# Kernel tuning notes

Measured on AMD Instinct MI355X. Metric: run time of the kernel, lower is better.

## Reference

```python
import jax, jax.numpy as jnp
import numpy as np

D_MODEL = 1024
NUM_HEADS = 16
THETA = 10000.0


def _trunc_normal(key, shape):
    # matches torch.nn.init.trunc_normal_(std=std, a=-3*std, b=3*std)
    std = (2.0 / (shape[0] + shape[1])) ** 0.5
    return jax.random.truncated_normal(key, -3.0, 3.0, shape, dtype=jnp.float32) * std


def setup_inputs() -> dict:
    key = jax.random.key(0)
    kx, kq, kk, kv, ko = jax.random.split(key, 5)
    B, S, D = 2, 2048, D_MODEL
    return {
        "x": jax.random.normal(kx, (B, S, D), dtype=jnp.float32),
        "Wq": _trunc_normal(kq, (D, D)),  # torch Linear weight: [out, in]
        "Wk": _trunc_normal(kk, (D, D)),
        "Wv": _trunc_normal(kv, (D, D)),
        "Wo": _trunc_normal(ko, (D, D)),
        "token_positions": jnp.arange(S, dtype=jnp.int32),
    }


def _rope(x, token_positions):
    # x: [B, H, S, d_k]; RoPE on interleaved pairs (k r) with r=2
    d_k = x.shape[-1]
    inv_freq = THETA ** (-2.0 * jnp.arange(d_k // 2, dtype=jnp.float32) / d_k)
    ang = token_positions.astype(jnp.float32)[:, None] * inv_freq[None, :]  # [S, d_k/2]
    sin, cos = jnp.sin(ang).astype(x.dtype), jnp.cos(ang).astype(x.dtype)
    x0, x1 = x[..., 0::2], x[..., 1::2]
    y0 = x0 * cos - x1 * sin
    y1 = x0 * sin + x1 * cos
    return jnp.stack([y0, y1], axis=-1).reshape(x.shape)


def reference(x, Wq, Wk, Wv, Wo, token_positions):
    B, S, D = x.shape
    H = NUM_HEADS
    d_k = D // H

    def proj(W):  # y = x @ W^T, split heads -> [B, H, S, d_k]
        y = jnp.einsum('bsd,ed->bse', x, W)
        return y.reshape(B, S, H, d_k).transpose(0, 2, 1, 3)

    q = _rope(proj(Wq), token_positions)
    k = _rope(proj(Wk), token_positions)
    v = proj(Wv)

    # causal mask: attend where pos_k <= pos_q
    mask = token_positions[None, :] <= token_positions[:, None]  # [S_q, S_k]
    logits = jnp.einsum('bhqd,bhkd->bhqk', q, k) / (d_k ** 0.5)
    logits = jnp.where(mask, logits, -jnp.inf)
    scores = jax.nn.softmax(logits, axis=-1)
    attn = jnp.einsum('bhqk,bhkd->bhqd', scores, v)  # [B, H, S, d_k]
    attn = attn.transpose(0, 2, 1, 3).reshape(B, S, D)
    return jnp.einsum('bsd,ed->bse', attn, Wo)
```

## Files before the change

kernel.cpp:

```cpp
#include <hip/hip_runtime.h>
#include <hip/hip_bf16.h>

typedef __attribute__((ext_vector_type(8))) short s16x8;
typedef __attribute__((ext_vector_type(4))) float f32x4;

__device__ __forceinline__ unsigned short f2b(float x) {
  unsigned int u = __float_as_uint(x);
  u = (u + 0x7fffu + ((u >> 16) & 1u)) >> 16;
  return (unsigned short)u;
}

__device__ __forceinline__ float b2f(unsigned short u) {
  return __uint_as_float((unsigned int)u << 16);
}

__device__ __forceinline__ unsigned int cvtpk(float a, float b) {
  unsigned int r;
  asm("v_cvt_pk_bf16_f32 %0, %1, %2" : "=v"(r) : "v"(a), "v"(b));
  return r;
}

#if __has_builtin(__builtin_amdgcn_exp2f)
__device__ __forceinline__ float fexp2(float x) { return __builtin_amdgcn_exp2f(x); }
#else
__device__ __forceinline__ float fexp2(float x) { return exp2f(x); }
#endif

__device__ __forceinline__ void gl2lds16(const unsigned short* g, unsigned short* lds) {
  __builtin_amdgcn_global_load_lds(
      (const __attribute__((address_space(1))) unsigned int*)g,
      (__attribute__((address_space(3))) unsigned int*)lds, 16, 0, 0);
}

#define QSCALE 0.18033688011f

__global__ __launch_bounds__(256) void cast_all(
    const float* __restrict__ x,  const float* __restrict__ Wq,
    const float* __restrict__ Wk, const float* __restrict__ Wv,
    const float* __restrict__ Wo, unsigned short* __restrict__ dst,
    float2* __restrict__ tbl) {
  const int blk = blockIdx.x;
  if (blk >= 8192) {
    int idx = (blk - 8192) * 256 + threadIdx.x;
    int s = idx >> 5, d2 = idx & 31;
    float inv = __expf(-0.2878231366f * (float)d2);
    float ang = (float)s * inv;
    float sn, cs;
    __sincosf(ang, &sn, &cs);
    tbl[idx] = make_float2(cs, sn);
    return;
  }
  int i = blk * 256 + threadIdx.x;
  const float* src;
  int off;
  if (i < 1048576) { src = x; off = i; }
  else {
    int j = i - 1048576;
    int seg = j >> 18;
    off = j & 262143;
    src = (seg == 0) ? Wq : (seg == 1) ? Wk : (seg == 2) ? Wv : Wo;
  }
  const float4 v = ((const float4*)src)[off];
  uint2 o;
  o.x = cvtpk(v.x, v.y);
  o.y = cvtpk(v.z, v.w);
  ((uint2*)dst)[i] = o;
}

#define KDIM 1024

__global__ __launch_bounds__(256, 4) void gemm_qkv(
    const unsigned short* __restrict__ A,
    const unsigned short* __restrict__ Bt,
    const int* __restrict__ tok,
    unsigned short* __restrict__ Qo,
    unsigned short* __restrict__ Ko,
    unsigned short* __restrict__ Vt,
    const float2* __restrict__ tbl) {
  __shared__ unsigned short As[2][128 * 32];
  __shared__ unsigned short Bs[2][128 * 32];
  const int tid = threadIdx.x;
  const int bid = blockIdx.x;
  const int xcd = bid & 7;
  const int loc = bid >> 3;
  const int m0 = (loc / 3) * 128;
  const int n0 = (xcd * 3 + loc % 3) * 128;
  const int w = tid >> 6, lane = tid & 63;
  const int ln = lane & 15, quad = lane >> 4;
  const int wm = (w >> 1) * 64, wn = (w & 1) * 64;

  const int rr = lane >> 2;
  const int gsw = ((lane & 3) ^ ((rr ^ (rr >> 2)) & 3)) * 8;
  const int sr = (ln ^ (ln >> 2)) & 3;

  const f32x4 zero = {0.f, 0.f, 0.f, 0.f};
  f32x4 acc[4][4];
#pragma unroll
  for (int i = 0; i < 4; ++i)
#pragma unroll
    for (int j = 0; j < 4; ++j) acc[i][j] = zero;

#define QKV_STAGE(kb, p)                                                              \
  do {                                                                                \
    int col = (kb) * 32 + gsw;                                                        \
    gl2lds16(A  + (size_t)(m0 + w * 32 + rr) * KDIM + col,      &As[p][(w * 32) * 32]);      \
    gl2lds16(A  + (size_t)(m0 + w * 32 + 16 + rr) * KDIM + col, &As[p][(w * 32 + 16) * 32]); \
    gl2lds16(Bt + (size_t)(n0 + w * 32 + rr) * KDIM + col,      &Bs[p][(w * 32) * 32]);      \
    gl2lds16(Bt + (size_t)(n0 + w * 32 + 16 + rr) * KDIM + col, &Bs[p][(w * 32 + 16) * 32]); \
  } while (0)

  QKV_STAGE(0, 0);
  for (int kb = 0; kb < 32; ++kb) {
    const int p = kb & 1;
    __syncthreads();
    if (kb < 31) QKV_STAGE(kb + 1, p ^ 1);
    s16x8 af[4], bfr[4];
#pragma unroll
    for (int i = 0; i < 4; ++i)
      af[i] = *(const s16x8*)(&As[p][(wm + i * 16 + ln) * 32 + ((quad ^ sr) * 8)]);
#pragma unroll
    for (int j = 0; j < 4; ++j)
      bfr[j] = *(const s16x8*)(&Bs[p][(wn + j * 16 + ln) * 32 + ((quad ^ sr) * 8)]);
#pragma unroll
    for (int i = 0; i < 4; ++i)
#pragma unroll
      for (int j = 0; j < 4; ++j)
        acc[i][j] = __builtin_amdgcn_mfma_f32_16x16x32_bf16(af[i], bfr[j], acc[i][j], 0, 0, 0);
  }
#undef QKV_STAGE

  const bool isV = (n0 >= 2048);
  if (!isV) {
    const float qs = (n0 < 1024) ? QSCALE : 1.0f;
#pragma unroll
    for (int j = 0; j < 4; ++j) {
      int gn = n0 + wn + j * 16 + ln;
      int e = gn & 1023;
      int h = e >> 6, d = e & 63;
      float inv = __expf(-0.2878231366f * (float)(d >> 1));
      unsigned short* dst = (gn < 1024) ? Qo : Ko;
#pragma unroll
      for (int i = 0; i < 4; ++i) {
        int gmb = m0 + wm + i * 16 + quad * 4;
#pragma unroll
        for (int r = 0; r < 4; ++r) {
          float val = acc[i][j][r];
          float part = __shfl_xor(val, 1, 64);
          int m = gmb + r;
          int b = m >> 11, s = m & 2047;
          float sn, cs;
          if (tbl) {
            float2 t = tbl[(s << 5) + (d >> 1)];
            cs = t.x; sn = t.y;
          } else {
            float ang = (float)s * inv;
            __sincosf(ang, &sn, &cs);
          }
          float x0 = (d & 1) ? part : val;
          float x1 = (d & 1) ? val : part;
          float y = (d & 1) ? (x0 * sn + x1 * cs) : (x0 * cs - x1 * sn);
          dst[(((size_t)b * 16 + h) * 2048 + s) * 64 + d] = f2b(y * qs);
        }
      }
    }
  } else {
    __syncthreads();
    unsigned short* T = &As[0][0] + w * 1120;
    const int b = m0 >> 11;
    const int hrow = ((n0 - 2048) + wn) >> 6;
    const int s0 = (m0 & 2047) + wm;
    const size_t vbase = (size_t)(b * 16 + hrow) * 64;
#pragma unroll
    for (int j = 0; j < 4; ++j) {
#pragma unroll
      for (int i = 0; i < 4; ++i)
#pragma unroll
        for (int r = 0; r < 4; ++r)
          T[ln * 70 + i * 16 + quad * 4 + r] = f2b(acc[i][j][r]);
      __builtin_amdgcn_wave_barrier();
#pragma unroll
      for (int dd = 0; dd < 16; ++dd)
        Vt[(vbase + j * 16 + dd) * 2048 + s0 + lane] = T[dd * 70 + lane];
      __builtin_amdgcn_wave_barrier();
    }
  }
}

__global__ __launch_bounds__(256, 3) void attn_partial(
    const unsigned short* __restrict__ Q,
    const unsigned short* __restrict__ K,
    const unsigned short* __restrict__ Vt,
    unsigned short* __restrict__ Opart,
    float2* __restrict__ ML) {
  __shared__ unsigned short Ks[2][64 * 64];
  __shared__ unsigned short Vs[2][64 * 64];
  __shared__ unsigned short Pt[4][16 * 72];

  const int bid = blockIdx.x;
  const int xcd = bid & 7;
  const int loc = bid >> 3;
  const int bh = xcd * 4 + (loc & 3);
  const int widx = loc >> 2;
  int c, qh;
  if (widx < 28) {
    if (widx < 13)      { c = 0; qh = 3 + widx; }
    else if (widx < 22) { c = 1; qh = 7 + (widx - 13); }
    else if (widx < 27) { c = 2; qh = 11 + (widx - 22); }
    else                { c = 3; qh = 15; }
  } else {
    int s = widx - 28;
    int wt = s >> 2;
    c = s & 3;
    qh = 4 * c + 2 - wt;
  }
  const int kbeg = c * 512;
  const int khi = min(kbeg + 512, qh * 128 + 128);
  const int nit = (khi - kbeg) >> 6;

  const int tid = threadIdx.x;
  const int w = tid >> 6, lane = tid & 63;
  const int ln = lane & 15, quad = lane >> 4;
  const int qb = qh * 128 + w * 32;

  const unsigned short* Qb = Q + (size_t)bh * 2048 * 64;
  const unsigned short* Kb = K + (size_t)bh * 2048 * 64;
  const unsigned short* Vb = Vt + (size_t)bh * 64 * 2048;

  const int srow = w * 16 + (lane >> 3);
  const int sg = (lane & 7) ^ (srow & 7);

#define ATTN_STAGE(k0, p)                                                            \
  do {                                                                               \
    gl2lds16(Kb + (size_t)((k0) + srow) * 64 + sg * 8,       &Ks[p][(w * 16) * 64]);      \
    gl2lds16(Kb + (size_t)((k0) + srow + 8) * 64 + sg * 8,   &Ks[p][(w * 16 + 8) * 64]);  \
    gl2lds16(Vb + (size_t)srow * 2048 + (k0) + sg * 8,       &Vs[p][(w * 16) * 64]);      \
    gl2lds16(Vb + (size_t)(srow + 8) * 2048 + (k0) + sg * 8, &Vs[p][(w * 16 + 8) * 64]);  \
  } while (0)

  s16x8 bq[2][2];
#pragma unroll
  for (int u = 0; u < 2; ++u)
#pragma unroll
    for (int hh = 0; hh < 2; ++hh)
      bq[u][hh] = *(const s16x8*)(&Qb[(size_t)(qb + u * 16 + ln) * 64 + hh * 32 + quad * 8]);

  const f32x4 zero = {0.f, 0.f, 0.f, 0.f};
  f32x4 o[2][4];
#pragma unroll
  for (int u = 0; u < 2; ++u)
#pragma unroll
    for (int j = 0; j < 4; ++j) o[u][j] = zero;
  float m_i[2] = {-3e38f, -3e38f};
  float l_i[2] = {0.f, 0.f};

  const int rdsw = ((ln & 7) * 8);

  ATTN_STAGE(kbeg, 0);
  for (int it = 0; it < nit; ++it) {
    const int p = it & 1;
    const int k0 = kbeg + it * 64;
    __syncthreads();
    if (it + 1 < nit) ATTN_STAGE(k0 + 64, p ^ 1);

    if (k0 <= qb + 31) {
      s16x8 ka[4][2];
#pragma unroll
      for (int t = 0; t < 4; ++t)
#pragma unroll
        for (int hh = 0; hh < 2; ++hh)
          ka[t][hh] = *(const s16x8*)(&Ks[p][(t * 16 + ln) * 64 + (((hh * 4 + quad) * 8) ^ rdsw)]);

#pragma unroll
      for (int u = 0; u < 2; ++u) {
        const int qlo = qb + u * 16;
        if (k0 > qlo + 15) continue;
        f32x4 st[4];
#pragma unroll
        for (int t = 0; t < 4; ++t) {
          f32x4 s = __builtin_amdgcn_mfma_f32_16x16x32_bf16(ka[t][0], bq[u][0], zero, 0, 0, 0);
          st[t] = __builtin_amdgcn_mfma_f32_16x16x32_bf16(ka[t][1], bq[u][1], s, 0, 0, 0);
        }
        float lm = -3e38f;
        if (k0 + 63 > qlo) {
          const int q = qlo + ln;
#pragma unroll
          for (int t = 0; t < 4; ++t)
#pragma unroll
            for (int r = 0; r < 4; ++r) {
              int kk = k0 + t * 16 + quad * 4 + r;
              float v = st[t][r];
              v = (kk > q) ? -3e38f : v;
              st[t][r] = v;
              lm = fmaxf(lm, v);
            }
        } else {
#pragma unroll
          for (int t = 0; t < 4; ++t)
#pragma unroll
            for (int r = 0; r < 4; ++r) lm = fmaxf(lm, st[t][r]);
        }
        lm = fmaxf(lm, __shfl_xor(lm, 16, 64));
        lm = fmaxf(lm, __shfl_xor(lm, 32, 64));

        float rs = 0.f;
        if (__all(lm <= m_i[u])) {
          const float mn = m_i[u];
#pragma unroll
          for (int t = 0; t < 4; ++t)
#pragma unroll
            for (int r = 0; r < 4; ++r) {
              float pv = fexp2(st[t][r] - mn);
              st[t][r] = pv;
              rs += pv;
            }
          rs += __shfl_xor(rs, 16, 64);
          rs += __shfl_xor(rs, 32, 64);
          l_i[u] += rs;
        } else {
          const float mn = fmaxf(m_i[u], lm);
          const float al = fexp2(m_i[u] - mn);
#pragma unroll
          for (int t = 0; t < 4; ++t)
#pragma unroll
            for (int r = 0; r < 4; ++r) {
              float pv = fexp2(st[t][r] - mn);
              st[t][r] = pv;
              rs += pv;
            }
          rs += __shfl_xor(rs, 16, 64);
          rs += __shfl_xor(rs, 32, 64);
          m_i[u] = mn;
          l_i[u] = l_i[u] * al + rs;
#pragma unroll
          for (int j = 0; j < 4; ++j) o[u][j] *= al;
        }

#pragma unroll
        for (int t = 0; t < 4; ++t) {
          uint2 pv;
          pv.x = cvtpk(st[t][0], st[t][1]);
          pv.y = cvtpk(st[t][2], st[t][3]);
          *(uint2*)(&Pt[w][ln * 72 + t * 16 + quad * 4]) = pv;
        }
        __builtin_amdgcn_wave_barrier();
#pragma unroll
        for (int hh = 0; hh < 2; ++hh) {
          s16x8 pb = *(const s16x8*)(&Pt[w][ln * 72 + hh * 32 + quad * 8]);
#pragma unroll
          for (int j = 0; j < 4; ++j) {
            s16x8 va = *(const s16x8*)(&Vs[p][(j * 16 + ln) * 64 + (((hh * 4 + quad) * 8) ^ rdsw)]);
            o[u][j] = __builtin_amdgcn_mfma_f32_16x16x32_bf16(va, pb, o[u][j], 0, 0, 0);
          }
        }
        __builtin_amdgcn_wave_barrier();
      }
    }
  }
#undef ATTN_STAGE

#pragma unroll
  for (int u = 0; u < 2; ++u) {
    int s = qb + u * 16 + ln;
    size_t row = ((size_t)bh * 4 + c) * 2048 + s;
    if (quad == 0) ML[row] = make_float2(m_i[u], l_i[u]);
    size_t base = row * 64;
#pragma unroll
    for (int j = 0; j < 4; ++j) {
      uint2 o4;
      o4.x = cvtpk(o[u][j][0], o[u][j][1]);
      o4.y = cvtpk(o[u][j][2], o[u][j][3]);
      *(uint2*)(&Opart[base + j * 16 + quad * 4]) = o4;
    }
  }
}

__global__ __launch_bounds__(256) void attn_merge(
    const unsigned short* __restrict__ Opart,
    const float2* __restrict__ ML,
    unsigned short* __restrict__ Ao) {
  int idx = blockIdx.x * 256 + threadIdx.x;
  int d0 = (idx & 7) * 8;
  int q  = (idx >> 3) & 2047;
  int bh = idx >> 14;
  int nc = (q >> 9) + 1;

  float m_c[4], l_c[4];
  float M = -3e38f;
  for (int c = 0; c < nc; ++c) {
    float2 ml = ML[((size_t)bh * 4 + c) * 2048 + q];
    m_c[c] = ml.x; l_c[c] = ml.y;
    M = fmaxf(M, ml.x);
  }
  float acc[8] = {0, 0, 0, 0, 0, 0, 0, 0};
  float L = 0.f;
  for (int c = 0; c < nc; ++c) {
    float wc = fexp2(m_c[c] - M);
    L += wc * l_c[c];
    const ushort4* p = (const ushort4*)(Opart + (((size_t)bh * 4 + c) * 2048 + q) * 64 + d0);
    ushort4 a = p[0], bvec = p[1];
    acc[0] += wc * b2f(a.x); acc[1] += wc * b2f(a.y);
    acc[2] += wc * b2f(a.z); acc[3] += wc * b2f(a.w);
    acc[4] += wc * b2f(bvec.x); acc[5] += wc * b2f(bvec.y);
    acc[6] += wc * b2f(bvec.z); acc[7] += wc * b2f(bvec.w);
  }
  float invL = 1.0f / L;
  int b = bh >> 4, h = bh & 15;
  unsigned short* dst = Ao + ((size_t)b * 2048 + q) * 1024 + h * 64 + d0;
  uint2 o0, o1;
  o0.x = cvtpk(acc[0] * invL, acc[1] * invL);
  o0.y = cvtpk(acc[2] * invL, acc[3] * invL);
  o1.x = cvtpk(acc[4] * invL, acc[5] * invL);
  o1.y = cvtpk(acc[6] * invL, acc[7] * invL);
  ((uint2*)dst)[0] = o0;
  ((uint2*)dst)[1] = o1;
}

__global__ __launch_bounds__(256, 3) void gemm_out(
    const unsigned short* __restrict__ A,
    const unsigned short* __restrict__ Bt,
    float* __restrict__ out) {
  __shared__ unsigned short As[128 * 64];
  __shared__ unsigned short Bs[128 * 64];
  const int tid = threadIdx.x;
  const int bid = blockIdx.x;
  const int m0 = (bid >> 3) * 128;
  const int n0 = (bid & 7) * 128;
  const int w = tid >> 6, lane = tid & 63;
  const int ln = lane & 15, quad = lane >> 4;
  const int wm = (w >> 1) * 64, wn = (w & 1) * 64;

  const int srow = w * 32 + (lane >> 3);
  const int sg = (lane & 7) ^ (lane >> 3);
  const int rs = ln & 7;

  const f32x4 zero = {0.f, 0.f, 0.f, 0.f};
  f32x4 acc[4][4];
#pragma unroll
  for (int i = 0; i < 4; ++i)
#pragma unroll
    for (int j = 0; j < 4; ++j) acc[i][j] = zero;

  for (int kb = 0; kb < KDIM / 64; ++kb) {
    __syncthreads();
#pragma unroll
    for (int t = 0; t < 4; ++t) {
      gl2lds16(A  + (size_t)(m0 + srow + t * 8) * KDIM + kb * 64 + sg * 8, &As[(w * 32 + t * 8) * 64]);
      gl2lds16(Bt + (size_t)(n0 + srow + t * 8) * KDIM + kb * 64 + sg * 8, &Bs[(w * 32 + t * 8) * 64]);
    }
    __syncthreads();
#pragma unroll
    for (int ks = 0; ks < 2; ++ks) {
      s16x8 af[4], bfr[4];
#pragma unroll
      for (int i = 0; i < 4; ++i)
        af[i] = *(const s16x8*)(&As[(wm + i * 16 + ln) * 64 + (((ks * 4 + quad) ^ rs) * 8)]);
#pragma unroll
      for (int j = 0; j < 4; ++j)
        bfr[j] = *(const s16x8*)(&Bs[(wn + j * 16 + ln) * 64 + (((ks * 4 + quad) ^ rs) * 8)]);
#pragma unroll
      for (int i = 0; i < 4; ++i)
#pragma unroll
        for (int j = 0; j < 4; ++j)
          acc[i][j] = __builtin_amdgcn_mfma_f32_16x16x32_bf16(af[i], bfr[j], acc[i][j], 0, 0, 0);
    }
  }
#pragma unroll
  for (int i = 0; i < 4; ++i) {
    int gmb = m0 + wm + i * 16 + quad * 4;
#pragma unroll
    for (int j = 0; j < 4; ++j) {
      int gn = n0 + wn + j * 16 + ln;
#pragma unroll
      for (int r = 0; r < 4; ++r)
        out[(size_t)(gmb + r) * 1024 + gn] = acc[i][j][r];
    }
  }
}

extern "C" void kernel_launch(void* const* d_in, const int* in_sizes, int n_in,
                              void* d_out, int out_size, void* d_ws, size_t ws_size,
                              hipStream_t stream) {
  const float* x  = (const float*)d_in[0];
  const float* Wq = (const float*)d_in[1];
  const float* Wk = (const float*)d_in[2];
  const float* Wv = (const float*)d_in[3];
  const float* Wo = (const float*)d_in[4];
  const int* tok  = (const int*)d_in[5];
  float* out = (float*)d_out;

  char* ws = (char*)d_ws;
  unsigned short* xb    = (unsigned short*)(ws);
  unsigned short* Wcat  = (unsigned short*)(ws + (8ull  << 20));
  unsigned short* Wob   = (unsigned short*)(ws + (14ull << 20));
  unsigned short* Qb    = (unsigned short*)(ws + (16ull << 20));
  unsigned short* Kb    = (unsigned short*)(ws + (24ull << 20));
  unsigned short* Vtb   = (unsigned short*)(ws + (32ull << 20));
  unsigned short* Ab    = (unsigned short*)(ws + (40ull << 20));
  unsigned short* Opart = (unsigned short*)(ws + (48ull << 20));
  float2*         ML    = (float2*)        (ws + (80ull << 20));
  float2* tbl = (ws_size >= (82ull << 20) + 65536 * sizeof(float2))
                    ? (float2*)(ws + (82ull << 20)) : (float2*)0;

  const int castGrid = tbl ? 8448 : 8192;
  cast_all<<<dim3(castGrid), dim3(256), 0, stream>>>(x, Wq, Wk, Wv, Wo, xb, tbl);
  gemm_qkv<<<dim3(768), dim3(256), 0, stream>>>(xb, Wcat, tok, Qb, Kb, Vtb, tbl);
  attn_partial<<<dim3(1280), dim3(256), 0, stream>>>(Qb, Kb, Vtb, Opart, ML);
  attn_merge<<<dim3(2048), dim3(256), 0, stream>>>(Opart, ML, Ab);
  gemm_out<<<dim3(256), dim3(256), 0, stream>>>(Ab, Wob, out);
}
```

Baseline: 198.5 us.

## Drop RoPE sin/cos table and stage Q/K epilogue through LDS for coalesced stores

Removes the precomputed sin/cos table built in the cast kernel and computes the RoPE angles inline with __sincosf in the QKV GEMM epilogue. The Q/K epilogue now writes rotated values into a per-wave LDS tile and then stores full 64-element rows, replacing the scattered 2-byte global stores. This removes the table's memory traffic and makes the Q/K writes coalesced, at the cost of more transcendental work per element and an extra LDS round trip.

```diff
diff --git a/kernel.cpp b/kernel.cpp
--- a/kernel.cpp
+++ b/kernel.cpp
@@ -37,20 +37,8 @@
 __global__ __launch_bounds__(256) void cast_all(
     const float* __restrict__ x,  const float* __restrict__ Wq,
     const float* __restrict__ Wk, const float* __restrict__ Wv,
-    const float* __restrict__ Wo, unsigned short* __restrict__ dst,
-    float2* __restrict__ tbl) {
-  const int blk = blockIdx.x;
-  if (blk >= 8192) {
-    int idx = (blk - 8192) * 256 + threadIdx.x;
-    int s = idx >> 5, d2 = idx & 31;
-    float inv = __expf(-0.2878231366f * (float)d2);
-    float ang = (float)s * inv;
-    float sn, cs;
-    __sincosf(ang, &sn, &cs);
-    tbl[idx] = make_float2(cs, sn);
-    return;
-  }
-  int i = blk * 256 + threadIdx.x;
+    const float* __restrict__ Wo, unsigned short* __restrict__ dst) {
+  int i = blockIdx.x * 256 + threadIdx.x;
   const float* src;
   int off;
   if (i < 1048576) { src = x; off = i; }
@@ -75,8 +63,7 @@
     const int* __restrict__ tok,
     unsigned short* __restrict__ Qo,
     unsigned short* __restrict__ Ko,
-    unsigned short* __restrict__ Vt,
-    const float2* __restrict__ tbl) {
+    unsigned short* __restrict__ Vt) {
   __shared__ unsigned short As[2][128 * 32];
   __shared__ unsigned short Bs[2][128 * 32];
   const int tid = threadIdx.x;
@@ -129,42 +116,48 @@
   }
 #undef QKV_STAGE
 
+  __syncthreads();
   const bool isV = (n0 >= 2048);
   if (!isV) {
-    const float qs = (n0 < 1024) ? QSCALE : 1.0f;
-#pragma unroll
-    for (int j = 0; j < 4; ++j) {
-      int gn = n0 + wn + j * 16 + ln;
-      int e = gn & 1023;
-      int h = e >> 6, d = e & 63;
-      float inv = __expf(-0.2878231366f * (float)(d >> 1));
-      unsigned short* dst = (gn < 1024) ? Qo : Ko;
-#pragma unroll
-      for (int i = 0; i < 4; ++i) {
-        int gmb = m0 + wm + i * 16 + quad * 4;
+    const float qs = (n0 + wn < 1024) ? QSCALE : 1.0f;
+    const int gnb = n0 + wn;
+    const int h = (gnb & 1023) >> 6;
+    unsigned short* dst = (gnb < 1024) ? Qo : Ko;
+    unsigned short* T = &As[0][0] + w * 1088;
+    float invj[4];
+#pragma unroll
+    for (int j = 0; j < 4; ++j)
+      invj[j] = __expf(-0.2878231366f * (float)((j * 16 + ln) >> 1));
+#pragma unroll
+    for (int i = 0; i < 4; ++i) {
+      const int mb = m0 + wm + i * 16;
+      const int b = mb >> 11;
+      const int sb = mb & 2047;
+#pragma unroll
+      for (int j = 0; j < 4; ++j) {
+        const int dd = j * 16 + ln;
 #pragma unroll
         for (int r = 0; r < 4; ++r) {
           float val = acc[i][j][r];
           float part = __shfl_xor(val, 1, 64);
-          int m = gmb + r;
-          int b = m >> 11, s = m & 2047;
+          int s = sb + quad * 4 + r;
+          float ang = (float)s * invj[j];
           float sn, cs;
-          if (tbl) {
-            float2 t = tbl[(s << 5) + (d >> 1)];
-            cs = t.x; sn = t.y;
-          } else {
-            float ang = (float)s * inv;
-            __sincosf(ang, &sn, &cs);
-          }
-          float x0 = (d & 1) ? part : val;
-          float x1 = (d & 1) ? val : part;
-          float y = (d & 1) ? (x0 * sn + x1 * cs) : (x0 * cs - x1 * sn);
-          dst[(((size_t)b * 16 + h) * 2048 + s) * 64 + d] = f2b(y * qs);
+          __sincosf(ang, &sn, &cs);
+          float x0 = (dd & 1) ? part : val;
+          float x1 = (dd & 1) ? val : part;
+          float y = (dd & 1) ? (x0 * sn + x1 * cs) : (x0 * cs - x1 * sn);
+          T[(quad * 4 + r) * 68 + dd] = f2b(y * qs);
         }
       }
+      __builtin_amdgcn_wave_barrier();
+      const size_t obase = ((size_t)(b * 16 + h) * 2048 + sb) * 64;
+#pragma unroll
+      for (int ss = 0; ss < 16; ++ss)
+        dst[obase + (size_t)ss * 64 + lane] = T[ss * 68 + lane];
+      __builtin_amdgcn_wave_barrier();
     }
   } else {
-    __syncthreads();
     unsigned short* T = &As[0][0] + w * 1120;
     const int b = m0 >> 11;
     const int hrow = ((n0 - 2048) + wn) >> 6;
@@ -498,12 +491,9 @@
   unsigned short* Ab    = (unsigned short*)(ws + (40ull << 20));
   unsigned short* Opart = (unsigned short*)(ws + (48ull << 20));
   float2*         ML    = (float2*)        (ws + (80ull << 20));
-  float2* tbl = (ws_size >= (82ull << 20) + 65536 * sizeof(float2))
-                    ? (float2*)(ws + (82ull << 20)) : (float2*)0;
-
-  const int castGrid = tbl ? 8448 : 8192;
-  cast_all<<<dim3(castGrid), dim3(256), 0, stream>>>(x, Wq, Wk, Wv, Wo, xb, tbl);
-  gemm_qkv<<<dim3(768), dim3(256), 0, stream>>>(xb, Wcat, tok, Qb, Kb, Vtb, tbl);
+
+  cast_all<<<dim3(8192), dim3(256), 0, stream>>>(x, Wq, Wk, Wv, Wo, xb);
+  gemm_qkv<<<dim3(768), dim3(256), 0, stream>>>(xb, Wcat, tok, Qb, Kb, Vtb);
   attn_partial<<<dim3(1280), dim3(256), 0, stream>>>(Qb, Kb, Vtb, Opart, ML);
   attn_merge<<<dim3(2048), dim3(256), 0, stream>>>(Opart, ML, Ab);
   gemm_out<<<dim3(256), dim3(256), 0, stream>>>(Ab, Wob, out);
```

After: 185.1 us. 6.7% less time.
